# Kernel tuning notes

Measured on AMD Instinct MI355X. Metric: run time of the kernel, lower is better.

The kernel has to match this reference:

```python
import jax, jax.numpy as jnp
import numpy as np

DIM, H, C = 1024, 16, 64
D = DIM // H  # head_dim = 64
GATE_HID = 16


def setup_inputs() -> dict:
    key = jax.random.key(0)
    ks = jax.random.split(key, 8)
    B, L = 2, 2048

    def xav(k, fan_in, fan_out):
        return jax.random.normal(k, (fan_in, fan_out), jnp.float32) * np.sqrt(2.0 / (fan_in + fan_out))

    return {
        "x": jax.random.normal(ks[0], (B, L, DIM), jnp.float32),
        "Wq": xav(ks[1], DIM, DIM), "bq": jnp.zeros((DIM,), jnp.float32),
        "Wk": xav(ks[2], DIM, DIM), "bk": jnp.zeros((DIM,), jnp.float32),
        "Wv": xav(ks[3], DIM, DIM), "bv": jnp.zeros((DIM,), jnp.float32),
        "Wg1": xav(ks[4], DIM, GATE_HID), "bg1": jnp.zeros((GATE_HID,), jnp.float32),
        "Wg2": xav(ks[5], GATE_HID, H * D), "bg2": jnp.zeros((H * D,), jnp.float32),
    }


def reference(x, Wq, bq, Wk, bk, Wv, bv, Wg1, bg1, Wg2, bg2):
    B, L, dim = x.shape
    pad = (-L) % C
    if pad:
        x = jnp.pad(x, ((0, 0), (0, pad), (0, 0)))
    Lp = L + pad

    def proj(W, b):
        # (B, Lp, dim) -> (B, H, Lp, D)
        return (x @ W + b).reshape(B, Lp, H, D).transpose(0, 2, 1, 3)

    q, k, v = proj(Wq, bq), proj(Wk, bk), proj(Wv, bv)
    gate = jax.nn.sigmoid(jax.nn.silu(x @ Wg1 + bg1) @ Wg2 + bg2)
    alpha = 0.9 * gate.reshape(B, Lp, H, D).transpose(0, 2, 1, 3) + 0.1  # (B,H,Lp,D)

    # --- intra-chunk causal softmax attention (vectorized over chunks) ---
    Nc = Lp // C
    qc = q.reshape(B, H, Nc, C, D)
    kc = k.reshape(B, H, Nc, C, D)
    vc = v.reshape(B, H, Nc, C, D)
    scores = jnp.einsum('bhncd,bhnkd->bhnck', qc, kc) / np.sqrt(D).astype(np.float32)
    causal = jnp.tril(jnp.ones((C, C), bool))
    scores = jnp.where(causal, scores, -jnp.inf)
    intra = jnp.einsum('bhnck,bhnke->bhnce', jax.nn.softmax(scores, axis=-1), vc)
    intra = intra.reshape(B, H, Lp, D)

    # --- inter: gated linear-attention recurrence over the full sequence ---
    # Note: in the original code S is updated every timestep (including inside
    # chunks), so the 'inter' term at step t sees ALL tokens < t, not just
    # previous chunks.
    def step(S, inp):
        q_t, k_t, v_t, a_t = inp  # each (B, H, D)
        inter_t = jnp.einsum('bhd,bhde->bhe', q_t, S)
        S = a_t[..., None] * S + k_t[..., None] * v_t[..., None, :]
        return S, inter_t

    xs = tuple(a.transpose(2, 0, 1, 3) for a in (q, k, v, alpha))  # (Lp, B, H, D)
    S0 = jnp.zeros((B, H, D, D), x.dtype)
    _, inter = jax.lax.scan(step, S0, xs)  # (Lp, B, H, D)
    inter = inter.transpose(1, 2, 0, 3)  # (B, H, Lp, D)

    out = (inter + intra).transpose(0, 2, 1, 3).reshape(B, Lp, dim)
    return out[:, :L]
```

## Files before the change

### kernel.cpp

```cpp
#include <hip/hip_runtime.h>
#include <math.h>

#define DIMN 1024
#define NH 16
#define HD 64
#define CHK 64
#define NB 2
#define SEQ 2048
#define NTOK (NB*SEQ)
#define NCHUNK (SEQ/CHK)
#define GH 16

typedef __bf16 bf16x8 __attribute__((ext_vector_type(8)));
typedef float f32x4 __attribute__((ext_vector_type(4)));
typedef unsigned short u16x4 __attribute__((ext_vector_type(4)));

__device__ __forceinline__ unsigned short f2bf(float f) {
  union { float f; unsigned u; } a; a.f = f;
  unsigned r = a.u + 0x7FFFu + ((a.u >> 16) & 1u);
  return (unsigned short)(r >> 16);
}
__device__ __forceinline__ float bf2f(unsigned short v) {
  union { unsigned u; float f; } a; a.u = ((unsigned)v) << 16;
  return a.f;
}

__device__ __forceinline__ void gload16(const void* g, void* l) {
  __builtin_amdgcn_global_load_lds(
      (const __attribute__((address_space(1))) void*)g,
      (__attribute__((address_space(3))) void*)l, 16, 0, 0);
}

__global__ __launch_bounds__(256) void k_cast_wT(const float* __restrict__ W0,
    const float* __restrict__ W1, const float* __restrict__ W2,
    unsigned short* __restrict__ wt) {
  __shared__ float tile[64][68];
  int z = blockIdx.z;
  const float* W = z==0 ? W0 : z==1 ? W1 : W2;
  unsigned short* o = wt + (size_t)z*DIMN*DIMN;
  int k0 = blockIdx.y*64, n0 = blockIdx.x*64;
  int tr = threadIdx.x >> 4, c0 = (threadIdx.x & 15)*4;
  #pragma unroll
  for (int s = 0; s < 4; ++s) {
    int r = tr + s*16;
    *(f32x4*)&tile[r][c0] = *(const f32x4*)(W + (size_t)(k0+r)*DIMN + n0 + c0);
  }
  __syncthreads();
  #pragma unroll
  for (int s = 0; s < 4; ++s) {
    int nn = tr + s*16;
    ushort4 v;
    v.x = f2bf(tile[c0+0][nn]);
    v.y = f2bf(tile[c0+1][nn]);
    v.z = f2bf(tile[c0+2][nn]);
    v.w = f2bf(tile[c0+3][nn]);
    *(ushort4*)(o + (size_t)(n0+nn)*DIMN + k0 + c0) = v;
  }
}

__global__ __launch_bounds__(256) void k_wg1t(const float* __restrict__ Wg1,
    unsigned short* __restrict__ wg1b) {
  int idx = blockIdx.x*256 + threadIdx.x;
  int k = idx & 1023, j = idx >> 10;
  wg1b[j*DIMN + k] = f2bf(Wg1[k*GH + j]);
}

__global__ __launch_bounds__(256) void k_castx_hidden(const float* __restrict__ x,
    const unsigned short* __restrict__ wg1b, const float* __restrict__ bg1,
    unsigned short* __restrict__ xb, float* __restrict__ hid) {
  __shared__ __align__(16) unsigned short xs[16][1032];
  __shared__ float red[4][16][16];
  int tid = threadIdx.x;
  size_t base = (size_t)blockIdx.x * 16 * DIMN;
  #pragma unroll
  for (int i = 0; i < 16; ++i) {
    int idx4 = tid + i*256;
    int r = idx4 >> 8, c4 = idx4 & 255;
    f32x4 v = *(const f32x4*)(x + base + (size_t)idx4*4);
    u16x4 o;
    o[0]=f2bf(v[0]); o[1]=f2bf(v[1]); o[2]=f2bf(v[2]); o[3]=f2bf(v[3]);
    *(u16x4*)&xs[r][c4*4] = o;
    *(u16x4*)(xb + base + (size_t)idx4*4) = o;
  }
  __syncthreads();
  int l = tid & 63, w = tid >> 6;
  int lr = l & 15, kg = l >> 4;
  union FB { uint4 u; bf16x8 h; } a, b;
  f32x4 acc = {0.f,0.f,0.f,0.f};
  const unsigned short* wrow = wg1b + (size_t)lr*DIMN + w*256 + kg*8;
  #pragma unroll
  for (int kk = 0; kk < 8; ++kk) {
    a.u = *(const uint4*)&xs[lr][w*256 + kk*32 + kg*8];
    b.u = *(const uint4*)(wrow + kk*32);
    acc = __builtin_amdgcn_mfma_f32_16x16x32_bf16(a.h, b.h, acc, 0, 0, 0);
  }
  #pragma unroll
  for (int rg = 0; rg < 4; ++rg) red[w][kg*4 + rg][lr] = acc[rg];
  __syncthreads();
  {
    int m = tid >> 4, j = tid & 15;
    float s = red[0][m][j] + red[1][m][j] + red[2][m][j] + red[3][m][j];
    s += bg1[j];
    hid[(blockIdx.x*16 + m)*GH + j] = s / (1.f + expf(-s));
  }
}

__global__ __launch_bounds__(256, 3) void k_projqkv(const unsigned short* __restrict__ xb,
    const unsigned short* __restrict__ wt,
    const float* __restrict__ b0, const float* __restrict__ b1, const float* __restrict__ b2,
    unsigned short* __restrict__ o0, unsigned short* __restrict__ o1,
    unsigned short* __restrict__ o2) {
  __shared__ unsigned short As[2][128*32];
  __shared__ unsigned short Bs[2][128*32];
  int tid = threadIdx.x;
  int wg = blockIdx.y * gridDim.x + blockIdx.x;
  int swz = (wg & 7) * 96 + (wg >> 3);
  int bx = swz % 24, by = swz / 24;
  int n3 = bx*128;
  int z = n3 >> 10;
  int n0l = n3 & 1023;
  const float* bias = z==0 ? b0 : z==1 ? b1 : b2;
  unsigned short* out = z==0 ? o0 : z==1 ? o1 : o2;
  int m0 = by*128;

  int l = tid & 63;
  int w = tid >> 6;
  int wr = w >> 1, wc = w & 1;
  int lrow = l & 15, kg = l >> 4;

  f32x4 acc[4][4] = {};

  int r0s = tid >> 2, s0s = tid & 3;
  int r1s = (tid + 256) >> 2;
  int sg0 = s0s ^ ((r0s >> 1) & 3);
  int sg1 = s0s ^ ((r1s >> 1) & 3);

  #define STAGE(buf, kt) do { \
    int kb_ = (kt)*32; \
    gload16(xb + ((size_t)(m0 + r0s)*DIMN + kb_ + sg0*8), &As[buf][tid*8]); \
    gload16(wt + ((size_t)(n3 + r0s)*DIMN + kb_ + sg0*8), &Bs[buf][tid*8]); \
    gload16(xb + ((size_t)(m0 + r1s)*DIMN + kb_ + sg1*8), &As[buf][(tid+256)*8]); \
    gload16(wt + ((size_t)(n3 + r1s)*DIMN + kb_ + sg1*8), &Bs[buf][(tid+256)*8]); \
  } while (0)

  STAGE(0, 0);
  int buf = 0;
  for (int t = 0; t < DIMN/32; ++t) {
    __syncthreads();
    if (t+1 < DIMN/32) STAGE(buf^1, t+1);
    union { uint4 u; bf16x8 h; } af[4], bfr[4];
    #pragma unroll
    for (int mf = 0; mf < 4; ++mf) {
      int r = wr*64 + mf*16 + lrow;
      int slot = kg ^ ((r >> 1) & 3);
      af[mf].u = *(const uint4*)&As[buf][r*32 + slot*8];
    }
    #pragma unroll
    for (int nf = 0; nf < 4; ++nf) {
      int r = wc*64 + nf*16 + lrow;
      int slot = kg ^ ((r >> 1) & 3);
      bfr[nf].u = *(const uint4*)&Bs[buf][r*32 + slot*8];
    }
    #pragma unroll
    for (int mf = 0; mf < 4; ++mf)
      #pragma unroll
      for (int nf = 0; nf < 4; ++nf)
        acc[mf][nf] = __builtin_amdgcn_mfma_f32_16x16x32_bf16(
            af[mf].h, bfr[nf].h, acc[mf][nf], 0, 0, 0);
    buf ^= 1;
  }
  #undef STAGE

  float bv[4];
  #pragma unroll
  for (int nf = 0; nf < 4; ++nf) bv[nf] = bias[n0l + wc*64 + nf*16 + lrow];
  #pragma unroll
  for (int mf = 0; mf < 4; ++mf) {
    int rbase = m0 + wr*64 + mf*16 + kg*4;
    #pragma unroll
    for (int nf = 0; nf < 4; ++nf) {
      int c = n0l + wc*64 + nf*16 + lrow;
      #pragma unroll
      for (int rg = 0; rg < 4; ++rg)
        out[(size_t)(rbase+rg)*DIMN + c] = f2bf(acc[mf][nf][rg] + bv[nf]);
    }
  }
}

__global__ __launch_bounds__(256, 3) void k_ginc(const unsigned short* __restrict__ kbuf,
    const unsigned short* __restrict__ vbuf,
    const float* __restrict__ hid, const float* __restrict__ Wg2,
    const float* __restrict__ bg2,
    unsigned short* __restrict__ G, float* __restrict__ Bv) {
  __shared__ __align__(16) unsigned short kb16[64*72];
  __shared__ __align__(16) unsigned short vT[64*72];
  __shared__ __align__(16) unsigned short kdT[64*72];
  __shared__ __align__(16) float scr[2048];
  __shared__ float seg[4][64];
  int tid = threadIdx.x;
  int bid = blockIdx.x;
  int bh = bid >> 5, n = bid & 31;
  int b = bh >> 4, h = bh & 15;
  int colbase = h*HD;
  size_t rowbase = (size_t)b*SEQ + n*CHK;

  {
    int r = tid >> 2, j0 = (tid & 3)*4;
    *(f32x4*)&scr[r*16 + j0] = *(const f32x4*)(hid + (rowbase + r)*GH + j0);
    int j = tid >> 4, d0 = (tid & 15)*4;
    *(f32x4*)&scr[1024 + j*64 + d0] = *(const f32x4*)(Wg2 + (size_t)j*DIMN + colbase + d0);
  }
  #pragma unroll
  for (int i = 0; i < 4; ++i) {
    int f4 = tid + i*256;
    int r = f4 >> 4, cg = f4 & 15, c0 = cg*4;
    size_t g = (rowbase + r)*DIMN + colbase + c0;
    u16x4 k4 = *(const u16x4*)(kbuf + g);
    u16x4 v4 = *(const u16x4*)(vbuf + g);
    *(u16x4*)&kb16[r*72 + c0] = k4;
    #pragma unroll
    for (int j = 0; j < 4; ++j) vT[(c0+j)*72 + r] = v4[j];
  }
  __syncthreads();

  {
    int d = tid & 63, ig = tid >> 6;
    float wcol[16];
    #pragma unroll
    for (int j = 0; j < 16; ++j) wcol[j] = scr[1024 + j*64 + d];
    float bgd = bg2[colbase + d];
    float P[16];
    float run = 0.f;
    #pragma unroll
    for (int t = 0; t < 16; ++t) {
      int i = ig*16 + t;
      float acc = bgd;
      #pragma unroll
      for (int j = 0; j < 16; ++j) acc = fmaf(scr[i*16 + j], wcol[j], acc);
      float gg = 1.f/(1.f + expf(-acc));
      run += log2f(fmaf(0.9f, gg, 0.1f));
      P[t] = run;
    }
    seg[ig][d] = run;
    __syncthreads();
    float s0 = seg[0][d], s1 = seg[1][d], s2 = seg[2][d], s3 = seg[3][d];
    float carry = (ig > 0 ? s0 : 0.f) + (ig > 1 ? s1 : 0.f) + (ig > 2 ? s2 : 0.f);
    float Lb63 = s0 + s1 + s2 + s3;
    if (ig == 0) Bv[(size_t)bid*HD + d] = exp2f(Lb63);
    union { unsigned short s[16]; uint4 u[2]; } kd;
    #pragma unroll
    for (int t = 0; t < 16; ++t) {
      int i = ig*16 + t;
      float kv = bf2f(kb16[i*72 + d]);
      kd.s[t] = f2bf(kv * exp2f(Lb63 - carry - P[t]));
    }
    *(uint4*)&kdT[d*72 + ig*16] = kd.u[0];
    *(uint4*)&kdT[d*72 + ig*16 + 8] = kd.u[1];
  }
  __syncthreads();

  int l = tid & 63, w = tid >> 6;
  int lr = l & 15, kg = l >> 4;
  int ks = kg*8;
  int arow = w*16 + lr;
  union FB { uint4 u; bf16x8 h; } a0, a1;
  a0.u = *(const uint4*)&kdT[arow*72 + ks];
  a1.u = *(const uint4*)&kdT[arow*72 + 32 + ks];
  unsigned short* gp = G + (size_t)bid*(HD*HD);
  #pragma unroll
  for (int nf = 0; nf < 4; ++nf) {
    FB b0v, b1v;
    b0v.u = *(const uint4*)&vT[(nf*16+lr)*72 + ks];
    b1v.u = *(const uint4*)&vT[(nf*16+lr)*72 + 32 + ks];
    f32x4 z = {0.f,0.f,0.f,0.f};
    z = __builtin_amdgcn_mfma_f32_16x16x32_bf16(a0.h, b0v.h, z, 0,0,0);
    z = __builtin_amdgcn_mfma_f32_16x16x32_bf16(a1.h, b1v.h, z, 0,0,0);
    #pragma unroll
    for (int rg = 0; rg < 4; ++rg)
      gp[(w*16 + kg*4 + rg)*HD + nf*16 + lr] = f2bf(z[rg]);
  }
}

__global__ __launch_bounds__(256) void k_scan(unsigned short* __restrict__ buf,
    const float* __restrict__ Bv) {
  int idx = blockIdx.x*256 + threadIdx.x;
  int e = idx & 63, d = (idx >> 6) & 63, bh = idx >> 12;
  unsigned short* gp = buf + (size_t)bh*NCHUNK*HD*HD + d*HD + e;
  const float* bp = Bv + (size_t)bh*NCHUNK*HD + d;
  float g[NCHUNK], bb[NCHUNK];
  #pragma unroll
  for (int n = 0; n < NCHUNK; ++n) g[n] = bf2f(gp[n*(HD*HD)]);
  #pragma unroll
  for (int n = 0; n < NCHUNK; ++n) bb[n] = bp[n*HD];
  float s = 0.f;
  #pragma unroll
  for (int n = 0; n < NCHUNK; ++n) {
    gp[n*(HD*HD)] = f2bf(s);
    s = fmaf(bb[n], s, g[n]);
  }
}

__global__ __launch_bounds__(256) void k_chunk(const unsigned short* __restrict__ qbuf,
    const unsigned short* __restrict__ kbuf, const unsigned short* __restrict__ vbuf,
    const float* __restrict__ hid, const float* __restrict__ Wg2,
    const float* __restrict__ bg2,
    const unsigned short* __restrict__ states, float* __restrict__ outp) {
  __shared__ __align__(16) unsigned short qb16[64*72];
  __shared__ __align__(16) unsigned short kb16[64*72];
  __shared__ __align__(16) unsigned short vT[64*72];
  __shared__ __align__(16) unsigned short Pl[64*72];
  __shared__ __align__(16) unsigned short Swt[2][64*72];
  __shared__ __align__(16) float lb[65*68];
  __shared__ __align__(16) unsigned short dgs[4][16*40];
  __shared__ float seg[4][64];

  const int tid = threadIdx.x;
  const int bid = blockIdx.x;
  const int bh = bid >> 5, n = bid & 31;
  const int b = bh >> 4, h = bh & 15;
  const int colbase = h*HD;
  const size_t rowbase = (size_t)b*SEQ + n*CHK;
  const unsigned short* stp = states + (size_t)(bh*NCHUNK + n)*(HD*HD);

  float* scr = (float*)Pl;
  {
    int r = tid >> 2, j0 = (tid & 3)*4;
    *(f32x4*)&scr[r*16 + j0] = *(const f32x4*)(hid + (rowbase + r)*GH + j0);
    int j = tid >> 4, d0 = (tid & 15)*4;
    *(f32x4*)&scr[1024 + j*64 + d0] = *(const f32x4*)(Wg2 + (size_t)j*DIMN + colbase + d0);
  }
  #pragma unroll
  for (int i = 0; i < 4; ++i) {
    int f4 = tid + i*256;
    int r = f4 >> 4, cg = f4 & 15, c0 = cg*4;
    size_t g = (rowbase + r)*DIMN + colbase + c0;
    u16x4 q4 = *(const u16x4*)(qbuf + g);
    u16x4 k4 = *(const u16x4*)(kbuf + g);
    u16x4 v4 = *(const u16x4*)(vbuf + g);
    u16x4 s4 = *(const u16x4*)(stp + r*HD + c0);
    #pragma unroll
    for (int j = 0; j < 4; ++j) {
      vT[(c0+j)*72 + r] = v4[j];
      Swt[0][(c0+j)*72 + r] = s4[j];
    }
    *(u16x4*)&qb16[r*72 + c0] = q4;
    *(u16x4*)&kb16[r*72 + c0] = k4;
  }
  __syncthreads();

  {
    int r = tid >> 2, db = (tid & 3)*16;
    float av[16];
    #pragma unroll
    for (int dq = 0; dq < 16; ++dq) {
      int d = db + dq;
      float acc = bg2[colbase + d];
      #pragma unroll
      for (int j = 0; j < GH; ++j)
        acc = fmaf(scr[r*16 + j], scr[1024 + j*64 + d], acc);
      float gg = 1.f/(1.f + expf(-acc));
      av[dq] = log2f(fmaf(0.9f, gg, 0.1f));
    }
    #pragma unroll
    for (int dq = 0; dq < 16; dq += 4) {
      f32x4 v4 = {av[dq], av[dq+1], av[dq+2], av[dq+3]};
      *(f32x4*)&lb[r*68 + db + dq] = v4;
    }
  }
  __syncthreads();

  {
    int d = tid & 63, ww = tid >> 6;
    float run = 0.f;
    #pragma unroll
    for (int ii = 0; ii < 16; ++ii) {
      int i = ww*16 + ii;
      float t = lb[i*68 + d];
      lb[i*68 + d] = run;
      run += t;
    }
    seg[ww][d] = run;
  }
  __syncthreads();
  {
    int d = tid & 63, ww = tid >> 6;
    float carry = 0.f;
    for (int w2 = 0; w2 < ww; ++w2) carry += seg[w2][d];
    if (ww > 0)
      for (int ii = 0; ii < 16; ++ii) lb[(ww*16+ii)*68 + d] += carry;
    if (ww == 3) lb[64*68 + d] = carry + seg[3][d];
  }
  __syncthreads();

  const int l = tid & 63, w = tid >> 6;
  const int lr = l & 15, lg = l >> 4;
  const int ks = lg*8;
  const int arow = w*16 + lr;

  union FB { uint4 u; bf16x8 h; unsigned short s[8]; };

  FB qa0, qa1;
  qa0.u = *(const uint4*)&qb16[arow*72 + ks];
  qa1.u = *(const uint4*)&qb16[arow*72 + 32 + ks];
  f32x4 sc[4];
  #pragma unroll
  for (int nf = 0; nf < 4; ++nf) {
    FB b0, b1;
    b0.u = *(const uint4*)&kb16[(nf*16+lr)*72 + ks];
    b1.u = *(const uint4*)&kb16[(nf*16+lr)*72 + 32 + ks];
    f32x4 z = {0.f,0.f,0.f,0.f};
    z = __builtin_amdgcn_mfma_f32_16x16x32_bf16(qa0.h, b0.h, z, 0,0,0);
    z = __builtin_amdgcn_mfma_f32_16x16x32_bf16(qa1.h, b1.h, z, 0,0,0);
    sc[nf] = z;
  }

  float rmax[4] = {-3e38f,-3e38f,-3e38f,-3e38f};
  #pragma unroll
  for (int nf = 0; nf < 4; ++nf) {
    int col = nf*16 + lr;
    #pragma unroll
    for (int rg = 0; rg < 4; ++rg) {
      int row = w*16 + lg*4 + rg;
      float v = sc[nf][rg]*0.125f;
      if (col > row) v = -1e30f;
      sc[nf][rg] = v;
      rmax[rg] = fmaxf(rmax[rg], v);
    }
  }
  #pragma unroll
  for (int m = 1; m <= 8; m <<= 1)
    #pragma unroll
    for (int rg = 0; rg < 4; ++rg)
      rmax[rg] = fmaxf(rmax[rg], __shfl_xor(rmax[rg], m));
  float rsum[4] = {0.f,0.f,0.f,0.f};
  #pragma unroll
  for (int nf = 0; nf < 4; ++nf)
    #pragma unroll
    for (int rg = 0; rg < 4; ++rg) {
      float e = exp2f((sc[nf][rg] - rmax[rg])*1.44269504f);
      sc[nf][rg] = e;
      rsum[rg] += e;
    }
  #pragma unroll
  for (int m = 1; m <= 8; m <<= 1)
    #pragma unroll
    for (int rg = 0; rg < 4; ++rg)
      rsum[rg] += __shfl_xor(rsum[rg], m);
  __syncthreads();
  #pragma unroll
  for (int nf = 0; nf < 4; ++nf)
    #pragma unroll
    for (int rg = 0; rg < 4; ++rg)
      Pl[(w*16 + lg*4 + rg)*72 + nf*16 + lr] = f2bf(sc[nf][rg]);
  float inv[4];
  #pragma unroll
  for (int rg = 0; rg < 4; ++rg) inv[rg] = 1.f/rsum[rg];
  __syncthreads();

  f32x4 acc[4];
  {
    FB p0, p1;
    p0.u = *(const uint4*)&Pl[arow*72 + ks];
    p1.u = *(const uint4*)&Pl[arow*72 + 32 + ks];
    #pragma unroll
    for (int nf = 0; nf < 4; ++nf) {
      FB v0, v1;
      v0.u = *(const uint4*)&vT[(nf*16+lr)*72 + ks];
      v1.u = *(const uint4*)&vT[(nf*16+lr)*72 + 32 + ks];
      f32x4 z = {0.f,0.f,0.f,0.f};
      z = __builtin_amdgcn_mfma_f32_16x16x32_bf16(p0.h, v0.h, z, 0,0,0);
      z = __builtin_amdgcn_mfma_f32_16x16x32_bf16(p1.h, v1.h, z, 0,0,0);
      #pragma unroll
      for (int rg = 0; rg < 4; ++rg)
        acc[nf][rg] = z[rg]*inv[rg];
    }
  }

  {
    int dA = arow;
    float lb32 = lb[32*68 + dA];
    FB ku;
    #pragma unroll
    for (int j = 0; j < 8; ++j) {
      int s = ks + j;
      float kv = bf2f(kb16[s*72 + dA]);
      ku.s[j] = f2bf(kv * exp2f(lb32 - lb[(s+1)*68 + dA]));
    }
    int d0 = w*16 + lg*4;
    float bs[4];
    #pragma unroll
    for (int rg = 0; rg < 4; ++rg) bs[rg] = exp2f(lb[32*68 + d0 + rg]);
    #pragma unroll
    for (int nf = 0; nf < 4; ++nf) {
      int e = nf*16 + lr;
      FB vv;
      vv.u = *(const uint4*)&vT[e*72 + ks];
      f32x4 z = {0.f,0.f,0.f,0.f};
      z = __builtin_amdgcn_mfma_f32_16x16x32_bf16(ku.h, vv.h, z, 0,0,0);
      u16x4 s0v = *(const u16x4*)&Swt[0][e*72 + d0];
      u16x4 s1v;
      #pragma unroll
      for (int rg = 0; rg < 4; ++rg)
        s1v[rg] = f2bf(z[rg] + bs[rg]*bf2f(s0v[rg]));
      *(u16x4*)&Swt[1][e*72 + d0] = s1v;
    }
  }
  __syncthreads();

  {
    const int T = (w >= 2) ? 32 : 0;
    const unsigned short* Ssel = (w >= 2) ? &Swt[1][0] : &Swt[0][0];
    FB qd[2];
    #pragma unroll
    for (int kst = 0; kst < 2; ++kst) {
      int ds = kst*32 + ks;
      f32x4 lbi0 = *(const f32x4*)&lb[arow*68 + ds];
      f32x4 lbi1 = *(const f32x4*)&lb[arow*68 + ds + 4];
      f32x4 lbt0 = *(const f32x4*)&lb[T*68 + ds];
      f32x4 lbt1 = *(const f32x4*)&lb[T*68 + ds + 4];
      FB qr;
      qr.u = *(const uint4*)&qb16[arow*72 + ds];
      #pragma unroll
      for (int j = 0; j < 4; ++j) {
        qd[kst].s[j]   = f2bf(bf2f(qr.s[j])   * exp2f(lbi0[j] - lbt0[j]));
        qd[kst].s[4+j] = f2bf(bf2f(qr.s[4+j]) * exp2f(lbi1[j] - lbt1[j]));
      }
    }
    #pragma unroll
    for (int nf = 0; nf < 4; ++nf) {
      FB s0f, s1f;
      s0f.u = *(const uint4*)&Ssel[(nf*16+lr)*72 + ks];
      s1f.u = *(const uint4*)&Ssel[(nf*16+lr)*72 + 32 + ks];
      acc[nf] = __builtin_amdgcn_mfma_f32_16x16x32_bf16(qd[0].h, s0f.h, acc[nf], 0,0,0);
      acc[nf] = __builtin_amdgcn_mfma_f32_16x16x32_bf16(qd[1].h, s1f.h, acc[nf], 0,0,0);
    }
    const int nb_ = (w & 1) ? 2 : 1;
    f32x4 dgc[2] = {{0.f,0.f,0.f,0.f},{0.f,0.f,0.f,0.f}};
    #pragma unroll
    for (int bf_ = 0; bf_ < 2; ++bf_) {
      if (bf_ < nb_) {
        int s = T + bf_*16 + lr;
        f32x4 z = {0.f,0.f,0.f,0.f};
        #pragma unroll
        for (int kst = 0; kst < 2; ++kst) {
          int ds = kst*32 + ks;
          f32x4 lbt0 = *(const f32x4*)&lb[T*68 + ds];
          f32x4 lbt1 = *(const f32x4*)&lb[T*68 + ds + 4];
          f32x4 lbs0 = *(const f32x4*)&lb[(s+1)*68 + ds];
          f32x4 lbs1 = *(const f32x4*)&lb[(s+1)*68 + ds + 4];
          FB kr, kd;
          kr.u = *(const uint4*)&kb16[s*72 + ds];
          #pragma unroll
          for (int j = 0; j < 4; ++j) {
            kd.s[j]   = f2bf(bf2f(kr.s[j])   * exp2f(lbt0[j] - lbs0[j]));
            kd.s[4+j] = f2bf(bf2f(kr.s[4+j]) * exp2f(lbt1[j] - lbs1[j]));
          }
          z = __builtin_amdgcn_mfma_f32_16x16x32_bf16(qd[kst].h, kd.h, z, 0,0,0);
        }
        dgc[bf_] = z;
      }
    }
    int iis = (w & 1)*16 + lg*4;
    #pragma unroll
    for (int bf_ = 0; bf_ < 2; ++bf_) {
      #pragma unroll
      for (int rg = 0; rg < 4; ++rg) {
        int ssu = bf_*16 + lr;
        float v = (bf_ < nb_ && ssu < iis + rg) ? dgc[bf_][rg] : 0.f;
        dgs[w][(lg*4 + rg)*40 + bf_*16 + lr] = f2bf(v);
      }
    }
    FB dga;
    dga.u = *(const uint4*)&dgs[w][lr*40 + ks];
    #pragma unroll
    for (int nf = 0; nf < 4; ++nf) {
      FB vv;
      vv.u = *(const uint4*)&vT[(nf*16+lr)*72 + T + ks];
      acc[nf] = __builtin_amdgcn_mfma_f32_16x16x32_bf16(dga.h, vv.h, acc[nf], 0,0,0);
    }
  }

  #pragma unroll
  for (int nf = 0; nf < 4; ++nf)
    #pragma unroll
    for (int rg = 0; rg < 4; ++rg)
      outp[(rowbase + w*16 + lg*4 + rg)*DIMN + colbase + nf*16 + lr] = acc[nf][rg];
}

extern "C" void kernel_launch(void* const* d_in, const int* in_sizes, int n_in,
                              void* d_out, int out_size, void* d_ws, size_t ws_size,
                              hipStream_t stream) {
  const float* x   = (const float*)d_in[0];
  const float* Wq  = (const float*)d_in[1];
  const float* bq  = (const float*)d_in[2];
  const float* Wk  = (const float*)d_in[3];
  const float* bk  = (const float*)d_in[4];
  const float* Wv  = (const float*)d_in[5];
  const float* bv  = (const float*)d_in[6];
  const float* Wg1 = (const float*)d_in[7];
  const float* bg1 = (const float*)d_in[8];
  const float* Wg2 = (const float*)d_in[9];
  const float* bg2 = (const float*)d_in[10];
  float* out = (float*)d_out;

  float* ws = (float*)d_ws;
  const size_t NT = (size_t)NTOK*DIMN;
  const size_t NST = (size_t)NB*NH*NCHUNK*HD*HD;
  float* hid = ws;
  float* Bv  = hid + (size_t)NTOK*GH;
  unsigned short* stb = (unsigned short*)(Bv + (size_t)NB*NH*NCHUNK*HD);
  unsigned short* xb = stb + NST;
  unsigned short* wt = xb + NT;
  unsigned short* wg1b = wt + 3*(size_t)DIMN*DIMN;
  unsigned short* qb = wg1b + (size_t)GH*DIMN;
  unsigned short* kb = qb + NT;
  unsigned short* vb = kb + NT;

  k_cast_wT<<<dim3(16, 16, 3), 256, 0, stream>>>(Wq, Wk, Wv, wt);
  k_wg1t<<<(GH*DIMN)/256, 256, 0, stream>>>(Wg1, wg1b);
  k_castx_hidden<<<NTOK/16, 256, 0, stream>>>(x, wg1b, bg1, xb, hid);
  k_projqkv<<<dim3(24, 32), 256, 0, stream>>>(
      xb, wt, bq, bk, bv, qb, kb, vb);
  k_ginc<<<NB*NH*NCHUNK, 256, 0, stream>>>(kb, vb, hid, Wg2, bg2, stb, Bv);
  k_scan<<<(NB*NH*HD*HD)/256, 256, 0, stream>>>(stb, Bv);
  k_chunk<<<NB*NH*NCHUNK, 256, 0, stream>>>(qb, kb, vb, hid, Wg2, bg2, stb, out);
}
```

Baseline: 94.70 us.

## Shrink k_chunk shared memory to raise occupancy, reading q/k from global

Removes the q and k shared tiles and the second state buffer, reading q/k fragments straight from global memory and writing the updated state in place between two phases. The gate projection is restructured so each thread computes a column and does its prefix scan in registers, merging two scan passes. Launch bounds request three blocks per CU. The goal is to cut LDS footprint and barriers so more blocks fit per CU, at the cost of extra global loads (uncoalesced transposed k reads), a serialized second inter phase for half the waves, and extra barriers.

```diff
diff --git a/kernel.cpp b/kernel.cpp
--- a/kernel.cpp
+++ b/kernel.cpp
@@ -300,19 +300,15 @@
   }
 }
 
-__global__ __launch_bounds__(256) void k_chunk(const unsigned short* __restrict__ qbuf,
+__global__ __launch_bounds__(256, 3) void k_chunk(const unsigned short* __restrict__ qbuf,
     const unsigned short* __restrict__ kbuf, const unsigned short* __restrict__ vbuf,
     const float* __restrict__ hid, const float* __restrict__ Wg2,
     const float* __restrict__ bg2,
     const unsigned short* __restrict__ states, float* __restrict__ outp) {
-  __shared__ __align__(16) unsigned short qb16[64*72];
-  __shared__ __align__(16) unsigned short kb16[64*72];
-  __shared__ __align__(16) unsigned short vT[64*72];
-  __shared__ __align__(16) unsigned short Pl[64*72];
-  __shared__ __align__(16) unsigned short Swt[2][64*72];
-  __shared__ __align__(16) float lb[65*68];
-  __shared__ __align__(16) unsigned short dgs[4][16*40];
-  __shared__ float seg[4][64];
+  __shared__ __align__(16) unsigned short vT[4600];
+  __shared__ __align__(16) unsigned short Swt[4600];
+  __shared__ __align__(16) unsigned short Pl[4608];
+  __shared__ __align__(16) float lb[4416];
 
   const int tid = threadIdx.x;
   const int bid = blockIdx.x;
@@ -323,72 +319,52 @@
   const unsigned short* stp = states + (size_t)(bh*NCHUNK + n)*(HD*HD);
 
   float* scr = (float*)Pl;
+  float* segp = scr + 1024;
+
   {
     int r = tid >> 2, j0 = (tid & 3)*4;
     *(f32x4*)&scr[r*16 + j0] = *(const f32x4*)(hid + (rowbase + r)*GH + j0);
-    int j = tid >> 4, d0 = (tid & 15)*4;
-    *(f32x4*)&scr[1024 + j*64 + d0] = *(const f32x4*)(Wg2 + (size_t)j*DIMN + colbase + d0);
   }
   #pragma unroll
   for (int i = 0; i < 4; ++i) {
     int f4 = tid + i*256;
     int r = f4 >> 4, cg = f4 & 15, c0 = cg*4;
-    size_t g = (rowbase + r)*DIMN + colbase + c0;
-    u16x4 q4 = *(const u16x4*)(qbuf + g);
-    u16x4 k4 = *(const u16x4*)(kbuf + g);
-    u16x4 v4 = *(const u16x4*)(vbuf + g);
+    u16x4 v4 = *(const u16x4*)(vbuf + (rowbase + r)*DIMN + colbase + c0);
     u16x4 s4 = *(const u16x4*)(stp + r*HD + c0);
     #pragma unroll
     for (int j = 0; j < 4; ++j) {
       vT[(c0+j)*72 + r] = v4[j];
-      Swt[0][(c0+j)*72 + r] = s4[j];
-    }
-    *(u16x4*)&qb16[r*72 + c0] = q4;
-    *(u16x4*)&kb16[r*72 + c0] = k4;
-  }
-  __syncthreads();
-
-  {
-    int r = tid >> 2, db = (tid & 3)*16;
-    float av[16];
-    #pragma unroll
-    for (int dq = 0; dq < 16; ++dq) {
-      int d = db + dq;
-      float acc = bg2[colbase + d];
-      #pragma unroll
-      for (int j = 0; j < GH; ++j)
-        acc = fmaf(scr[r*16 + j], scr[1024 + j*64 + d], acc);
+      Swt[(c0+j)*72 + r] = s4[j];
+    }
+  }
+  __syncthreads();
+
+  {
+    int d = tid & 63, ig = tid >> 6;
+    float wcol[16];
+    #pragma unroll
+    for (int j = 0; j < 16; ++j) wcol[j] = Wg2[(size_t)j*DIMN + colbase + d];
+    float bgd = bg2[colbase + d];
+    float Pex[16];
+    float run = 0.f;
+    #pragma unroll
+    for (int t = 0; t < 16; ++t) {
+      int i = ig*16 + t;
+      float acc = bgd;
+      #pragma unroll
+      for (int j = 0; j < 16; ++j) acc = fmaf(scr[i*16 + j], wcol[j], acc);
       float gg = 1.f/(1.f + expf(-acc));
-      av[dq] = log2f(fmaf(0.9f, gg, 0.1f));
-    }
-    #pragma unroll
-    for (int dq = 0; dq < 16; dq += 4) {
-      f32x4 v4 = {av[dq], av[dq+1], av[dq+2], av[dq+3]};
-      *(f32x4*)&lb[r*68 + db + dq] = v4;
-    }
-  }
-  __syncthreads();
-
-  {
-    int d = tid & 63, ww = tid >> 6;
-    float run = 0.f;
-    #pragma unroll
-    for (int ii = 0; ii < 16; ++ii) {
-      int i = ww*16 + ii;
-      float t = lb[i*68 + d];
-      lb[i*68 + d] = run;
-      run += t;
-    }
-    seg[ww][d] = run;
-  }
-  __syncthreads();
-  {
-    int d = tid & 63, ww = tid >> 6;
+      Pex[t] = run;
+      run += log2f(fmaf(0.9f, gg, 0.1f));
+    }
+    segp[ig*64 + d] = run;
+    __syncthreads();
     float carry = 0.f;
-    for (int w2 = 0; w2 < ww; ++w2) carry += seg[w2][d];
-    if (ww > 0)
-      for (int ii = 0; ii < 16; ++ii) lb[(ww*16+ii)*68 + d] += carry;
-    if (ww == 3) lb[64*68 + d] = carry + seg[3][d];
+    for (int w2 = 0; w2 < ig; ++w2) carry += segp[w2*64 + d];
+    #pragma unroll
+    for (int t = 0; t < 16; ++t)
+      lb[(ig*16 + t)*68 + d] = carry + Pex[t];
+    if (ig == 3) lb[64*68 + d] = carry + run;
   }
   __syncthreads();
 
@@ -399,15 +375,17 @@
 
   union FB { uint4 u; bf16x8 h; unsigned short s[8]; };
 
+  const unsigned short* qrow = qbuf + (rowbase + arow)*DIMN + colbase;
   FB qa0, qa1;
-  qa0.u = *(const uint4*)&qb16[arow*72 + ks];
-  qa1.u = *(const uint4*)&qb16[arow*72 + 32 + ks];
+  qa0.u = *(const uint4*)(qrow + ks);
+  qa1.u = *(const uint4*)(qrow + 32 + ks);
   f32x4 sc[4];
   #pragma unroll
   for (int nf = 0; nf < 4; ++nf) {
+    const unsigned short* krow = kbuf + (rowbase + nf*16 + lr)*DIMN + colbase;
     FB b0, b1;
-    b0.u = *(const uint4*)&kb16[(nf*16+lr)*72 + ks];
-    b1.u = *(const uint4*)&kb16[(nf*16+lr)*72 + 32 + ks];
+    b0.u = *(const uint4*)(krow + ks);
+    b1.u = *(const uint4*)(krow + 32 + ks);
     f32x4 z = {0.f,0.f,0.f,0.f};
     z = __builtin_amdgcn_mfma_f32_16x16x32_bf16(qa0.h, b0.h, z, 0,0,0);
     z = __builtin_amdgcn_mfma_f32_16x16x32_bf16(qa1.h, b1.h, z, 0,0,0);
@@ -446,7 +424,6 @@
     #pragma unroll
     for (int rg = 0; rg < 4; ++rg)
       rsum[rg] += __shfl_xor(rsum[rg], m);
-  __syncthreads();
   #pragma unroll
   for (int nf = 0; nf < 4; ++nf)
     #pragma unroll
@@ -476,6 +453,7 @@
     }
   }
 
+  u16x4 s1v[4];
   {
     int dA = arow;
     float lb32 = lb[32*68 + dA];
@@ -483,7 +461,7 @@
     #pragma unroll
     for (int j = 0; j < 8; ++j) {
       int s = ks + j;
-      float kv = bf2f(kb16[s*72 + dA]);
+      float kv = bf2f(kbuf[(rowbase + s)*DIMN + colbase + dA]);
       ku.s[j] = f2bf(kv * exp2f(lb32 - lb[(s+1)*68 + dA]));
     }
     int d0 = w*16 + lg*4;
@@ -497,19 +475,16 @@
       vv.u = *(const uint4*)&vT[e*72 + ks];
       f32x4 z = {0.f,0.f,0.f,0.f};
       z = __builtin_amdgcn_mfma_f32_16x16x32_bf16(ku.h, vv.h, z, 0,0,0);
-      u16x4 s0v = *(const u16x4*)&Swt[0][e*72 + d0];
-      u16x4 s1v;
+      u16x4 s0v = *(const u16x4*)&Swt[e*72 + d0];
       #pragma unroll
       for (int rg = 0; rg < 4; ++rg)
-        s1v[rg] = f2bf(z[rg] + bs[rg]*bf2f(s0v[rg]));
-      *(u16x4*)&Swt[1][e*72 + d0] = s1v;
-    }
-  }
-  __syncthreads();
-
-  {
-    const int T = (w >= 2) ? 32 : 0;
-    const unsigned short* Ssel = (w >= 2) ? &Swt[1][0] : &Swt[0][0];
+        s1v[nf][rg] = f2bf(z[rg] + bs[rg]*bf2f(s0v[rg]));
+    }
+  }
+  __syncthreads();
+
+  unsigned short* dgs = Pl;
+  auto do_inter = [&](int T) {
     FB qd[2];
     #pragma unroll
     for (int kst = 0; kst < 2; ++kst) {
@@ -518,8 +493,7 @@
       f32x4 lbi1 = *(const f32x4*)&lb[arow*68 + ds + 4];
       f32x4 lbt0 = *(const f32x4*)&lb[T*68 + ds];
       f32x4 lbt1 = *(const f32x4*)&lb[T*68 + ds + 4];
-      FB qr;
-      qr.u = *(const uint4*)&qb16[arow*72 + ds];
+      FB qr = (kst == 0) ? qa0 : qa1;
       #pragma unroll
       for (int j = 0; j < 4; ++j) {
         qd[kst].s[j]   = f2bf(bf2f(qr.s[j])   * exp2f(lbi0[j] - lbt0[j]));
@@ -529,8 +503,8 @@
     #pragma unroll
     for (int nf = 0; nf < 4; ++nf) {
       FB s0f, s1f;
-      s0f.u = *(const uint4*)&Ssel[(nf*16+lr)*72 + ks];
-      s1f.u = *(const uint4*)&Ssel[(nf*16+lr)*72 + 32 + ks];
+      s0f.u = *(const uint4*)&Swt[(nf*16+lr)*72 + ks];
+      s1f.u = *(const uint4*)&Swt[(nf*16+lr)*72 + 32 + ks];
       acc[nf] = __builtin_amdgcn_mfma_f32_16x16x32_bf16(qd[0].h, s0f.h, acc[nf], 0,0,0);
       acc[nf] = __builtin_amdgcn_mfma_f32_16x16x32_bf16(qd[1].h, s1f.h, acc[nf], 0,0,0);
     }
@@ -549,7 +523,7 @@
           f32x4 lbs0 = *(const f32x4*)&lb[(s+1)*68 + ds];
           f32x4 lbs1 = *(const f32x4*)&lb[(s+1)*68 + ds + 4];
           FB kr, kd;
-          kr.u = *(const uint4*)&kb16[s*72 + ds];
+          kr.u = *(const uint4*)(kbuf + (rowbase + s)*DIMN + colbase + ds);
           #pragma unroll
           for (int j = 0; j < 4; ++j) {
             kd.s[j]   = f2bf(bf2f(kr.s[j])   * exp2f(lbt0[j] - lbs0[j]));
@@ -567,18 +541,29 @@
       for (int rg = 0; rg < 4; ++rg) {
         int ssu = bf_*16 + lr;
         float v = (bf_ < nb_ && ssu < iis + rg) ? dgc[bf_][rg] : 0.f;
-        dgs[w][(lg*4 + rg)*40 + bf_*16 + lr] = f2bf(v);
+        dgs[w*640 + (lg*4 + rg)*40 + bf_*16 + lr] = f2bf(v);
       }
     }
     FB dga;
-    dga.u = *(const uint4*)&dgs[w][lr*40 + ks];
+    dga.u = *(const uint4*)&dgs[w*640 + lr*40 + ks];
     #pragma unroll
     for (int nf = 0; nf < 4; ++nf) {
       FB vv;
       vv.u = *(const uint4*)&vT[(nf*16+lr)*72 + T + ks];
       acc[nf] = __builtin_amdgcn_mfma_f32_16x16x32_bf16(dga.h, vv.h, acc[nf], 0,0,0);
     }
-  }
+  };
+
+  if (w < 2) do_inter(0);
+  __syncthreads();
+  {
+    int d0 = w*16 + lg*4;
+    #pragma unroll
+    for (int nf = 0; nf < 4; ++nf)
+      *(u16x4*)&Swt[(nf*16+lr)*72 + d0] = s1v[nf];
+  }
+  __syncthreads();
+  if (w >= 2) do_inter(32);
 
   #pragma unroll
   for (int nf = 0; nf < 4; ++nf)
```

Result: slower. 96.66 us (+2.1%).
